# Optimization experiments

Measured on AMD Instinct MI355X. Metric: run time of the kernel, lower is better.

Reference implementation:

```python
import jax, jax.numpy as jnp
import numpy as np
import math

N, E, R = 50000, 800000, 32
DIN = 128
H, D = 8, 16          # num_heads, head_dim; H*D == out_ent_feats == 128
HOP = 5
ALPHA = 0.1
EPS = 1e-5


def layer_norm(x, g, b):
    m = jnp.mean(x, axis=-1, keepdims=True)
    v = jnp.mean((x - m) ** 2, axis=-1, keepdims=True)
    return (x - m) * jax.lax.rsqrt(v + EPS) * g + b


def segment_softmax(e, dst, num_nodes):
    # e: [E, H] scores, softmax over incoming edges of each dst node
    m = jax.ops.segment_max(e, dst, num_segments=num_nodes)      # [N, H]
    ex = jnp.exp(e - m[dst])
    s = jax.ops.segment_sum(ex, dst, num_segments=num_nodes)     # [N, H]
    return ex / s[dst]


def setup_inputs() -> dict:
    key = jax.random.key(0)
    ks = jax.random.split(key, 12)
    gain = 0.02  # small init scale (small_init_gain-style)
    ent_feat = jax.random.normal(ks[0], (N, DIN), dtype=jnp.float32)
    rel_feat = jax.random.normal(ks[1], (R, DIN), dtype=jnp.float32)
    src = jax.random.randint(ks[2], (E,), 0, N, dtype=jnp.int32)
    # guarantee every node has in-degree >= 1 (DGL raises otherwise)
    dst_rand = jax.random.randint(ks[3], (E - N,), 0, N, dtype=jnp.int32)
    dst = jnp.concatenate([jnp.arange(N, dtype=jnp.int32), dst_rand])
    rid = jax.random.randint(ks[4], (E,), 0, R, dtype=jnp.int32)
    W_head = jax.random.normal(ks[5], (DIN, H * D), dtype=jnp.float32) * gain
    W_tail = jax.random.normal(ks[6], (DIN, H * D), dtype=jnp.float32) * gain
    W_ent = jax.random.normal(ks[7], (DIN, H * D), dtype=jnp.float32) * gain
    W_rel = jax.random.normal(ks[8], (DIN, H * D), dtype=jnp.float32) * gain
    attn_r = jax.random.normal(ks[9], (1, H, D), dtype=jnp.float32) * gain
    W1 = jax.random.normal(ks[10], (H * D, 4 * H * D), dtype=jnp.float32) * gain
    W2 = jax.random.normal(ks[11], (4 * H * D, H * D), dtype=jnp.float32) * gain
    return dict(
        ent_feat=ent_feat, rel_feat=rel_feat, src=src, dst=dst, rid=rid,
        W_head=W_head, W_tail=W_tail, W_ent=W_ent, W_rel=W_rel, attn_r=attn_r,
        ln_ent_g=jnp.ones((DIN,), jnp.float32), ln_ent_b=jnp.zeros((DIN,), jnp.float32),
        ln_rel_g=jnp.ones((DIN,), jnp.float32), ln_rel_b=jnp.zeros((DIN,), jnp.float32),
        ff_ln_g=jnp.ones((H * D,), jnp.float32), ff_ln_b=jnp.zeros((H * D,), jnp.float32),
        W1=W1, b1=jnp.zeros((4 * H * D,), jnp.float32),
        W2=W2, b2=jnp.zeros((H * D,), jnp.float32),
    )


def _forward(ent_feat, rel_feat, src, dst, rid,
             W_head, W_tail, W_ent, W_rel, attn_r,
             ln_ent_g, ln_ent_b, ln_rel_g, ln_rel_b, ff_ln_g, ff_ln_b,
             W1, b1, W2, b2):
    n = ent_feat.shape[0]
    x = layer_norm(ent_feat, ln_ent_g, ln_ent_b)
    feat_head = (x @ W_head).reshape(n, H, D)
    feat_tail = (x @ W_tail).reshape(n, H, D)
    feat_ent = (x @ W_ent).reshape(n, H, D)

    # per-edge dot-product attention score: u_dot_v('eh','et')
    e = jnp.sum(feat_head[src] * feat_tail[dst], axis=-1)          # [E, H]

    r = layer_norm(rel_feat, ln_rel_g, ln_rel_b)
    feat_rel = (r @ W_rel).reshape(R, H, D)
    er = jnp.sum(feat_rel * attn_r, axis=-1)                       # [R, H]
    e = e * er[rid]                                                # [E, H]

    # e_mul_v with log_in = log(in_degree) of dst node
    deg = jax.ops.segment_sum(jnp.ones((e.shape[0],), e.dtype), dst, num_segments=n)
    log_in = jnp.log(jnp.maximum(deg, 1.0))                        # [N]
    e = e * log_in[dst][:, None] / math.sqrt(D)

    a = segment_softmax(e, dst, n)                                 # [E, H]

    # PPR diffusion: feat <- (1-alpha) * A^T feat + alpha * feat_0
    feat = feat_ent
    for _ in range(HOP):
        msg = feat[src] * a[:, :, None]                            # [E, H, D]
        agg = jax.ops.segment_sum(msg, dst, num_segments=n)        # [N, H, D]
        feat = (1.0 - ALPHA) * agg + ALPHA * feat_ent

    # residual (Identity: in_ent_feats == out_ent_feats)
    rst = feat + ent_feat.reshape(n, H, D)
    rst = rst.reshape(n, H * D)

    h = layer_norm(rst, ff_ln_g, ff_ln_b)
    ff = jax.nn.relu(h @ W1 + b1) @ W2 + b2
    return ff + rst


def reference(ent_feat, rel_feat, src, dst, rid,
              W_head, W_tail, W_ent, W_rel, attn_r,
              ln_ent_g, ln_ent_b, ln_rel_g, ln_rel_b, ff_ln_g, ff_ln_b,
              W1, b1, W2, b2):
    return _forward(ent_feat, rel_feat, src, dst, rid,
                    W_head, W_tail, W_ent, W_rel, attn_r,
                    ln_ent_g, ln_ent_b, ln_rel_g, ln_rel_b, ff_ln_g, ff_ln_b,
                    W1, b1, W2, b2)
```

## Files before the change

kernel.cpp:

```cpp
#include <hip/hip_runtime.h>
#include <hip/hip_bf16.h>

#define N_NODES 50000
#define N_EDGES 800000
#define N_REL 32
#define DIN 128
#define NH 8
#define HD 16
#define FF_HID 512
#define EPS_LN 1e-5f
#define NBUCK 8
#define BDIV 6250
#define BCAP 114688

typedef __attribute__((ext_vector_type(8))) short bf16x8;
typedef __attribute__((ext_vector_type(4))) float f32x4;
typedef __attribute__((ext_vector_type(2))) float f32x2;
typedef unsigned short ushort_t;
typedef unsigned int uint_t;

static __device__ __forceinline__ unsigned short f2bf(float f) {
    union { float f; unsigned u; } v; v.f = f;
    unsigned r = (v.u + 0x7fffu + ((v.u >> 16) & 1u)) >> 16;
    return (unsigned short)r;
}
static __device__ __forceinline__ float bf2f(unsigned u16) {
    union { unsigned u; float f; } v; v.u = u16 << 16; return v.f;
}
static __device__ __forceinline__ unsigned char f2fp8(float f) {
    return (unsigned char)(__builtin_amdgcn_cvt_pk_fp8_f32(f, f, 0, false) & 0xff);
}
static __device__ __forceinline__ uint_t f2fp8x2(float x0, float x1) {
    return (__builtin_amdgcn_cvt_pk_fp8_f32(x0, x1, 0, false) & 0xffffu);
}
static __device__ __forceinline__ void fp8x4_to_f32(uint_t w, float* o) {
    f32x2 lo = __builtin_amdgcn_cvt_pk_f32_fp8(w, false);
    f32x2 hi = __builtin_amdgcn_cvt_pk_f32_fp8(w, true);
    o[0] = lo.x; o[1] = lo.y; o[2] = hi.x; o[3] = hi.y;
}

static __device__ __forceinline__ void pack_dev(const float* __restrict__ W,
                                                short* __restrict__ out, int K, int Ncols,
                                                int idx) {
    int KT = K >> 5;
    int l = idx & 63;
    int tile = idx >> 6;
    int kt = tile & (KT - 1);
    int ct = tile / KT;
    int c = ct * 16 + (l & 15);
    int k0 = kt * 32 + ((l >> 4) * 8);
    bf16x8 v;
#pragma unroll
    for (int j = 0; j < 8; j++) v[j] = (short)f2bf(W[(size_t)(k0 + j) * Ncols + c]);
    *(bf16x8*)(out + (size_t)idx * 8) = v;
}

#define C0_BIN 512
__global__ __launch_bounds__(256) void combo0_kernel(
    const int* __restrict__ src, const int* __restrict__ dst, const int* __restrict__ rid,
    int* __restrict__ deg, int* __restrict__ gcnt, int2* __restrict__ buck,
    const float* __restrict__ W1, short* __restrict__ W1p, const float* __restrict__ W2,
    short* __restrict__ W2p, const float* __restrict__ Wh, short* __restrict__ Whp,
    const float* __restrict__ Wt, short* __restrict__ Wtp, const float* __restrict__ We,
    short* __restrict__ Wep, const float* __restrict__ rel_feat,
    const float* __restrict__ gr, const float* __restrict__ br,
    const float* __restrict__ W_rel, const float* __restrict__ attn_r,
    float* __restrict__ er) {
    __shared__ float red[128];
    __shared__ float xsr[128];
    __shared__ float prod[128];
    __shared__ int cnt[NBUCK];
    __shared__ int sbase[NBUCK];
    int b = blockIdx.x, tid = threadIdx.x;
    if (b < C0_BIN) {
        const int chunk = (N_EDGES + C0_BIN - 1) / C0_BIN;
        int i0 = b * chunk;
        int i1 = min(i0 + chunk, N_EDGES);
        int rounds = (i1 - i0 + 255) >> 8;
        for (int r = 0; r < rounds; r++) {
            int i = i0 + (r << 8) + tid;
            if (tid < NBUCK) cnt[tid] = 0;
            __syncthreads();
            int d = 0, b8 = 0, rank = 0, py = 0;
            bool v = i < i1;
            if (v) {
                d = dst[i];
                b8 = d / BDIV;
                py = src[i] | (rid[i] << 16);
                rank = atomicAdd(&cnt[b8], 1);
                atomicAdd(&deg[d], 1);
            }
            __syncthreads();
            if (tid < NBUCK) sbase[tid] = atomicAdd(&gcnt[tid], cnt[tid]);
            __syncthreads();
            if (v) buck[(size_t)b8 * BCAP + sbase[b8] + rank] = make_int2(d, py);
            __syncthreads();
        }
    } else if (b < C0_BIN + 32) {
        pack_dev(W1, W1p, DIN, FF_HID, (b - C0_BIN) * 256 + tid);
    } else if (b < C0_BIN + 64) {
        pack_dev(W2, W2p, FF_HID, DIN, (b - C0_BIN - 32) * 256 + tid);
    } else if (b < C0_BIN + 72) {
        pack_dev(Wh, Whp, DIN, DIN, (b - C0_BIN - 64) * 256 + tid);
    } else if (b < C0_BIN + 80) {
        pack_dev(Wt, Wtp, DIN, DIN, (b - C0_BIN - 72) * 256 + tid);
    } else if (b < C0_BIN + 88) {
        pack_dev(We, Wep, DIN, DIN, (b - C0_BIN - 80) * 256 + tid);
    } else {
        int r = b - (C0_BIN + 88);
        float x = 0.f;
        if (tid < 128) {
            x = rel_feat[r * DIN + tid];
            red[tid] = x;
        }
        __syncthreads();
        for (int off = 64; off > 0; off >>= 1) {
            if (tid < off) red[tid] += red[tid + off];
            __syncthreads();
        }
        float mean = red[0] * (1.f / DIN);
        __syncthreads();
        if (tid < 128) red[tid] = x * x;
        __syncthreads();
        for (int off = 64; off > 0; off >>= 1) {
            if (tid < off) red[tid] += red[tid + off];
            __syncthreads();
        }
        float var = red[0] * (1.f / DIN) - mean * mean;
        float rs = rsqrtf(var + EPS_LN);
        if (tid < 128) xsr[tid] = (x - mean) * rs * gr[tid] + br[tid];
        __syncthreads();
        if (tid < 128) {
            float acc = 0.f;
            for (int k = 0; k < DIN; k++) acc += xsr[k] * W_rel[k * DIN + tid];
            prod[tid] = acc * attn_r[tid];
        }
        __syncthreads();
        if (tid < NH) {
            float s = 0.f;
            for (int d = 0; d < HD; d++) s += prod[tid * HD + d];
            er[r * NH + tid] = s;
        }
    }
}

#define NS_SCAN 196
__global__ __launch_bounds__(256) void combo_mid_kernel(
    const int* __restrict__ deg, int* __restrict__ row_off,
    const float* __restrict__ ent, const float* __restrict__ g, const float* __restrict__ b,
    const short* __restrict__ Whp, const short* __restrict__ Wtp,
    const short* __restrict__ Wep, unsigned char* __restrict__ hent,
    ushort_t* __restrict__ tail_bf) {
    __shared__ float xs[32][128];
    __shared__ short hsb[32][136];
    int blk = blockIdx.x, tid = threadIdx.x;
    if (blk < NS_SCAN) {
        __shared__ int lscan[256];
        __shared__ int ws4[4];
        int n = N_NODES;
        int start = blk * 256;
        int partial = 0;
        for (int i = tid; i < start; i += 256) partial += deg[i];
        for (int m = 32; m > 0; m >>= 1) partial += __shfl_down(partial, m);
        int wid = tid >> 6, lane = tid & 63;
        if (lane == 0) ws4[wid] = partial;
        __syncthreads();
        int sbase = ws4[0] + ws4[1] + ws4[2] + ws4[3];
        int i = start + tid;
        int v = (i < n) ? deg[i] : 0;
        lscan[tid] = v;
        __syncthreads();
        for (int off = 1; off < 256; off <<= 1) {
            int t = (tid >= off) ? lscan[tid - off] : 0;
            __syncthreads();
            lscan[tid] += t;
            __syncthreads();
        }
        if (i < n) row_off[i] = sbase + lscan[tid] - v;
        if (i == n - 1) row_off[n] = sbase + lscan[tid];
        return;
    }
    int base = (blk - NS_SCAN) * 32;
    {
        int c = tid & 127, rb = tid >> 7;
#pragma unroll
        for (int j = 0; j < 16; j++) {
            int r = j * 2 + rb;
            int row = base + r;
            xs[r][c] = (row < N_NODES) ? ent[(size_t)row * DIN + c] : 0.f;
        }
    }
    __syncthreads();
    int wave = tid >> 6, lane = tid & 63;
    {
        float g0 = g[lane], g1 = g[lane + 64], bb0 = b[lane], bb1 = b[lane + 64];
        for (int r = wave * 8; r < wave * 8 + 8; r++) {
            float x0 = xs[r][lane], x1 = xs[r][lane + 64];
            float s1 = x0 + x1, s2 = x0 * x0 + x1 * x1;
            for (int m = 1; m < 64; m <<= 1) {
                s1 += __shfl_xor(s1, m);
                s2 += __shfl_xor(s2, m);
            }
            float mean = s1 * (1.f / DIN);
            float var = s2 * (1.f / DIN) - mean * mean;
            float rs = rsqrtf(var + EPS_LN);
            hsb[r][lane] = (short)f2bf((x0 - mean) * rs * g0 + bb0);
            hsb[r][lane + 64] = (short)f2bf((x1 - mean) * rs * g1 + bb1);
        }
    }
    __syncthreads();
    bf16x8 a[2][4];
#pragma unroll
    for (int rt = 0; rt < 2; rt++)
#pragma unroll
        for (int kt = 0; kt < 4; kt++)
            a[rt][kt] = *(const bf16x8*)&hsb[rt * 16 + (lane & 15)][kt * 32 + (lane >> 4) * 8];
#pragma unroll
    for (int m = 0; m < 3; m++) {
        const bf16x8* bp = (m == 0)   ? (const bf16x8*)Whp
                           : (m == 1) ? (const bf16x8*)Wtp
                                      : (const bf16x8*)Wep;
#pragma unroll
        for (int c2 = 0; c2 < 2; c2++) {
            int ct = wave * 2 + c2;
            f32x4 acc0 = {0.f, 0.f, 0.f, 0.f}, acc1 = {0.f, 0.f, 0.f, 0.f};
#pragma unroll
            for (int kt = 0; kt < 4; kt++) {
                bf16x8 bf = bp[(ct * 4 + kt) * 64 + lane];
                acc0 = __builtin_amdgcn_mfma_f32_16x16x32_bf16(a[0][kt], bf, acc0, 0, 0, 0);
                acc1 = __builtin_amdgcn_mfma_f32_16x16x32_bf16(a[1][kt], bf, acc1, 0, 0, 0);
            }
            int col = ct * 16 + (lane & 15);
            int h = col >> 4, k = col & 15;
            int r0 = (lane >> 4) * 4;
#pragma unroll
            for (int j = 0; j < 4; j++) {
                int row0 = base + r0 + j, row1 = base + 16 + r0 + j;
                if (m == 0) {
                    if (row0 < N_NODES) hent[(size_t)row0 * 256 + h * 32 + k] = f2fp8(acc0[j]);
                    if (row1 < N_NODES) hent[(size_t)row1 * 256 + h * 32 + k] = f2fp8(acc1[j]);
                } else if (m == 1) {
                    if (row0 < N_NODES) tail_bf[(size_t)row0 * DIN + col] = f2bf(acc0[j]);
                    if (row1 < N_NODES) tail_bf[(size_t)row1 * DIN + col] = f2bf(acc1[j]);
                } else {
                    if (row0 < N_NODES)
                        hent[(size_t)row0 * 256 + h * 32 + 16 + k] = f2fp8(acc0[j]);
                    if (row1 < N_NODES)
                        hent[(size_t)row1 * 256 + h * 32 + 16 + k] = f2fp8(acc1[j]);
                }
            }
        }
    }
}

__global__ __launch_bounds__(256) void scatter_kernel(
    const int2* __restrict__ buck, const int* __restrict__ gcnt,
    const int* __restrict__ row_off, int* __restrict__ cursor, int* __restrict__ sr_perm) {
    int blk = blockIdx.x, tid = threadIdx.x;
    int b8 = blk & 7, sub = blk >> 3;
    int cnt = gcnt[b8];
    int chunk = (cnt + 127) >> 7;
    int i0 = sub * chunk;
    int i1 = min(i0 + chunk, cnt);
    const int2* bp = buck + (size_t)b8 * BCAP;
    for (int i = i0 + tid; i < i1; i += 256) {
        int2 e = bp[i];
        int p = row_off[e.x] + atomicAdd(&cursor[e.x], 1);
        sr_perm[p] = e.y;
    }
}

__global__ __launch_bounds__(256) void score_hop_kernel(
    const unsigned char* __restrict__ hent, const ushort_t* __restrict__ tail_bf,
    const float* __restrict__ er, const int* __restrict__ row_off,
    const int* __restrict__ sr_perm, ushort_t* __restrict__ a_bf,
    float* __restrict__ inv9, unsigned char* __restrict__ fout) {
    int wid = threadIdx.x >> 6;
    int u = blockIdx.x * 4 + wid;
    int lane = threadIdx.x & 63;
    int h = lane & 7, esub = lane >> 3;
    int p0 = row_off[u], p1 = row_off[u + 1];
    int deg = p1 - p0;
    float scale = logf((float)(deg > 0 ? deg : 1)) * 0.25f;
    float t[16];
    {
        const uint_t* tp = (const uint_t*)(tail_bf + (size_t)u * DIN + h * HD);
#pragma unroll
        for (int i = 0; i < 8; i++) {
            uint_t w = tp[i];
            t[2 * i] = bf2f(w & 0xffffu);
            t[2 * i + 1] = bf2f(w >> 16);
        }
    }
    float ssum = 0.f;
    float acc[16];
#pragma unroll
    for (int k = 0; k < 16; k++) acc[k] = 0.f;
    for (int p = p0 + esub; p < p1; p += 8) {
        int v = sr_perm[p];
        int s = v & 0xffff;
        int rr = v >> 16;
        const uint4* hp = (const uint4*)(hent + (size_t)s * 256 + h * 32);
        uint4 hw = hp[0];
        uint4 ew = hp[1];
        float hv[16], ev[16];
        fp8x4_to_f32(hw.x, hv + 0); fp8x4_to_f32(hw.y, hv + 4);
        fp8x4_to_f32(hw.z, hv + 8); fp8x4_to_f32(hw.w, hv + 12);
        fp8x4_to_f32(ew.x, ev + 0); fp8x4_to_f32(ew.y, ev + 4);
        fp8x4_to_f32(ew.z, ev + 8); fp8x4_to_f32(ew.w, ev + 12);
        float dot = 0.f;
#pragma unroll
        for (int k = 0; k < 16; k++) dot += t[k] * hv[k];
        float e = dot * er[rr * NH + h] * scale;
        float sx = expf(e);
        a_bf[(size_t)p * NH + h] = f2bf(sx);
        ssum += sx;
#pragma unroll
        for (int k = 0; k < 16; k++) acc[k] += sx * ev[k];
    }
    ssum += __shfl_xor(ssum, 8);
    ssum += __shfl_xor(ssum, 16);
    ssum += __shfl_xor(ssum, 32);
#pragma unroll
    for (int k = 0; k < 16; k++) {
        acc[k] += __shfl_xor(acc[k], 8);
        acc[k] += __shfl_xor(acc[k], 16);
        acc[k] += __shfl_xor(acc[k], 32);
    }
    if (esub == 0) {
        float iv = 0.9f / ssum;
        inv9[(size_t)u * NH + h] = iv;
        const uint4 eu = *(const uint4*)(hent + (size_t)u * 256 + h * 32 + 16);
        float e0[16];
        fp8x4_to_f32(eu.x, e0 + 0); fp8x4_to_f32(eu.y, e0 + 4);
        fp8x4_to_f32(eu.z, e0 + 8); fp8x4_to_f32(eu.w, e0 + 12);
        float x[16];
#pragma unroll
        for (int k = 0; k < 16; k++) x[k] = iv * acc[k] + 0.1f * e0[k];
        uint4 ov;
        ov.x = f2fp8x2(x[0], x[1]) | (f2fp8x2(x[2], x[3]) << 16);
        ov.y = f2fp8x2(x[4], x[5]) | (f2fp8x2(x[6], x[7]) << 16);
        ov.z = f2fp8x2(x[8], x[9]) | (f2fp8x2(x[10], x[11]) << 16);
        ov.w = f2fp8x2(x[12], x[13]) | (f2fp8x2(x[14], x[15]) << 16);
        *(uint4*)(fout + (size_t)u * DIN + h * HD) = ov;
    }
}

template <bool OUT_BF>
__global__ __launch_bounds__(256) void diffuse4_kernel(
    const unsigned char* __restrict__ fin8, const unsigned char* __restrict__ hent,
    const ushort_t* __restrict__ a_bf, const int* __restrict__ sr_perm,
    const int* __restrict__ row_off, const float* __restrict__ inv9,
    void* __restrict__ fout) {
    int wid = threadIdx.x >> 6;
    int u = blockIdx.x * 4 + wid;
    int lane = threadIdx.x & 63;
    int c = lane & 15;
    int g = lane >> 4;
    int hh = c >> 1;
    int p0 = row_off[u], p1 = row_off[u + 1];
    float acc[8];
#pragma unroll
    for (int j = 0; j < 8; j++) acc[j] = 0.f;
    for (int p = p0; p < p1; p += 4) {
        int pe = p + g;
        bool valid = pe < p1;
        int pc = valid ? pe : (p1 - 1);
        int s = sr_perm[pc] & 0xffff;
        float a = valid ? bf2f(a_bf[(size_t)pc * NH + hh]) : 0.f;
        uint2 w = *(const uint2*)(fin8 + (size_t)s * DIN + 8 * c);
        float v[8];
        fp8x4_to_f32(w.x, v + 0);
        fp8x4_to_f32(w.y, v + 4);
#pragma unroll
        for (int j = 0; j < 8; j++) acc[j] += a * v[j];
    }
#pragma unroll
    for (int j = 0; j < 8; j++) {
        acc[j] += __shfl_xor(acc[j], 16);
        acc[j] += __shfl_xor(acc[j], 32);
    }
    if (g == 0) {
        float iv = inv9[(size_t)u * NH + hh];
        uint2 ew = *(const uint2*)(hent + (size_t)u * 256 + hh * 32 + 16 + (c & 1) * 8);
        float e0[8];
        fp8x4_to_f32(ew.x, e0 + 0);
        fp8x4_to_f32(ew.y, e0 + 4);
        float x[8];
#pragma unroll
        for (int j = 0; j < 8; j++) x[j] = iv * acc[j] + 0.1f * e0[j];
        size_t o = (size_t)u * DIN + 8 * c;
        if (OUT_BF) {
            uint4 ov;
            ov.x = (uint_t)f2bf(x[0]) | ((uint_t)f2bf(x[1]) << 16);
            ov.y = (uint_t)f2bf(x[2]) | ((uint_t)f2bf(x[3]) << 16);
            ov.z = (uint_t)f2bf(x[4]) | ((uint_t)f2bf(x[5]) << 16);
            ov.w = (uint_t)f2bf(x[6]) | ((uint_t)f2bf(x[7]) << 16);
            *(uint4*)((ushort_t*)fout + o) = ov;
        } else {
            uint2 ov;
            ov.x = f2fp8x2(x[0], x[1]) | (f2fp8x2(x[2], x[3]) << 16);
            ov.y = f2fp8x2(x[4], x[5]) | (f2fp8x2(x[6], x[7]) << 16);
            *(uint2*)((unsigned char*)fout + o) = ov;
        }
    }
}

static __device__ __forceinline__ int hid_idx(int row, int col) {
    return row * 512 + ((((col >> 3) & 63) ^ (row & 7)) << 3) + (col & 7);
}
__global__ __launch_bounds__(256) void ffn_mfma_kernel(
    const ushort_t* __restrict__ feat, const float* __restrict__ ent0,
    const float* __restrict__ g, const float* __restrict__ b,
    const short* __restrict__ W1p, const float* __restrict__ b1,
    const short* __restrict__ W2p, const float* __restrict__ b2,
    float* __restrict__ out) {
    __shared__ ushort_t rst_bf[16][136];
    __shared__ short hs[16][136];
    __shared__ short hid[16 * 512];
    int tid = threadIdx.x;
    int base = blockIdx.x * 16;
    int wave = tid >> 6, lane = tid & 63;
    {
        int c = tid & 127, rb = tid >> 7;
#pragma unroll
        for (int j = 0; j < 8; j++) {
            int r = j * 2 + rb;
            int row = base + r;
            float v = 0.f;
            if (row < N_NODES) {
                size_t idx = (size_t)row * DIN + c;
                v = bf2f(feat[idx]) + ent0[idx];
            }
            rst_bf[r][c] = f2bf(v);
        }
    }
    __syncthreads();
    {
        float g0 = g[lane], g1 = g[lane + 64], bb0 = b[lane], bb1 = b[lane + 64];
        for (int r = wave * 4; r < wave * 4 + 4; r++) {
            float x0 = bf2f(rst_bf[r][lane]), x1 = bf2f(rst_bf[r][lane + 64]);
            float s1 = x0 + x1, s2 = x0 * x0 + x1 * x1;
            for (int m = 1; m < 64; m <<= 1) {
                s1 += __shfl_xor(s1, m);
                s2 += __shfl_xor(s2, m);
            }
            float mean = s1 * (1.f / DIN);
            float var = s2 * (1.f / DIN) - mean * mean;
            float rs = rsqrtf(var + EPS_LN);
            hs[r][lane] = (short)f2bf((x0 - mean) * rs * g0 + bb0);
            hs[r][lane + 64] = (short)f2bf((x1 - mean) * rs * g1 + bb1);
        }
    }
    __syncthreads();
    {
        bf16x8 a[4];
#pragma unroll
        for (int kt = 0; kt < 4; kt++)
            a[kt] = *(const bf16x8*)&hs[lane & 15][kt * 32 + (lane >> 4) * 8];
        const bf16x8* bp = (const bf16x8*)W1p;
        for (int cti = 0; cti < 8; cti++) {
            int ct = wave * 8 + cti;
            f32x4 acc0 = {0.f, 0.f, 0.f, 0.f};
#pragma unroll
            for (int kt = 0; kt < 4; kt++) {
                bf16x8 bf = bp[(ct * 4 + kt) * 64 + lane];
                acc0 = __builtin_amdgcn_mfma_f32_16x16x32_bf16(a[kt], bf, acc0, 0, 0, 0);
            }
            int col = ct * 16 + (lane & 15);
            float bv = b1[col];
            int r0 = (lane >> 4) * 4;
#pragma unroll
            for (int j = 0; j < 4; j++)
                hid[hid_idx(r0 + j, col)] = (short)f2bf(fmaxf(acc0[j] + bv, 0.f));
        }
    }
    __syncthreads();
    {
        f32x4 acc[2] = {{0.f, 0.f, 0.f, 0.f}, {0.f, 0.f, 0.f, 0.f}};
        const bf16x8* bp2 = (const bf16x8*)W2p;
        for (int kt = 0; kt < 16; kt++) {
            int col8 = kt * 32 + (lane >> 4) * 8;
            bf16x8 a0 = *(const bf16x8*)&hid[hid_idx(lane & 15, col8)];
#pragma unroll
            for (int c2 = 0; c2 < 2; c2++) {
                int ct = wave * 2 + c2;
                bf16x8 bf = bp2[(ct * 16 + kt) * 64 + lane];
                acc[c2] = __builtin_amdgcn_mfma_f32_16x16x32_bf16(a0, bf, acc[c2], 0, 0, 0);
            }
        }
#pragma unroll
        for (int c2 = 0; c2 < 2; c2++) {
            int col = (wave * 2 + c2) * 16 + (lane & 15);
            float bv = b2[col];
            int r0 = (lane >> 4) * 4;
#pragma unroll
            for (int j = 0; j < 4; j++) {
                int row = base + r0 + j;
                if (row < N_NODES)
                    out[(size_t)row * DIN + col] = acc[c2][j] + bv + bf2f(rst_bf[r0 + j][col]);
            }
        }
    }
}

extern "C" void kernel_launch(void* const* d_in, const int* in_sizes, int n_in,
                              void* d_out, int out_size, void* d_ws, size_t ws_size,
                              hipStream_t stream) {
    const float* ent_feat = (const float*)d_in[0];
    const float* rel_feat = (const float*)d_in[1];
    const int* src = (const int*)d_in[2];
    const int* dst = (const int*)d_in[3];
    const int* rid = (const int*)d_in[4];
    const float* W_head = (const float*)d_in[5];
    const float* W_tail = (const float*)d_in[6];
    const float* W_ent = (const float*)d_in[7];
    const float* W_rel = (const float*)d_in[8];
    const float* attn_r = (const float*)d_in[9];
    const float* ln_ent_g = (const float*)d_in[10];
    const float* ln_ent_b = (const float*)d_in[11];
    const float* ln_rel_g = (const float*)d_in[12];
    const float* ln_rel_b = (const float*)d_in[13];
    const float* ff_ln_g = (const float*)d_in[14];
    const float* ff_ln_b = (const float*)d_in[15];
    const float* W1 = (const float*)d_in[16];
    const float* b1 = (const float*)d_in[17];
    const float* W2 = (const float*)d_in[18];
    const float* b2 = (const float*)d_in[19];
    float* out = (float*)d_out;

    const int N = N_NODES, E = N_EDGES;

    char* cur = (char*)d_ws;
    auto alloc = [&](size_t bytes, size_t align) -> void* {
        uintptr_t p = (uintptr_t)cur;
        p = (p + align - 1) & ~(uintptr_t)(align - 1);
        cur = (char*)(p + bytes);
        return (void*)p;
    };
    ushort_t* tail_bf = (ushort_t*)alloc((size_t)N * DIN * 2, 16);
    unsigned char* hent = (unsigned char*)alloc((size_t)N * 256, 16);
    unsigned char* f8A = (unsigned char*)alloc((size_t)N * DIN, 16);
    unsigned char* f8B = (unsigned char*)alloc((size_t)N * DIN, 16);
    int2* buck = (int2*)alloc((size_t)NBUCK * BCAP * 8, 16);
    int* sr_perm = (int*)alloc((size_t)E * 4, 16);
    int* row_off = (int*)alloc((size_t)(N + 1) * 4, 16);
    int* deg = (int*)alloc(((size_t)2 * N + NBUCK) * 4, 16);
    int* cursor = deg + N;
    int* gcnt = deg + 2 * N;
    float* er = (float*)alloc((size_t)N_REL * NH * 4, 16);
    float* inv9 = (float*)alloc((size_t)N * NH * 4, 16);
    short* W1p = (short*)alloc((size_t)DIN * FF_HID * 2, 16);
    short* W2p = (short*)alloc((size_t)FF_HID * DIN * 2, 16);
    short* Whp = (short*)alloc((size_t)DIN * DIN * 2, 16);
    short* Wtp = (short*)alloc((size_t)DIN * DIN * 2, 16);
    short* Wep = (short*)alloc((size_t)DIN * DIN * 2, 16);
    ushort_t* a_fit = (ushort_t*)alloc((size_t)E * NH * 2, 16);
    ushort_t* a_bf = ((size_t)(cur - (char*)d_ws) <= ws_size) ? a_fit : (ushort_t*)d_out;

    hipMemsetAsync(deg, 0, sizeof(int) * ((size_t)2 * N + NBUCK), stream);
    combo0_kernel<<<632, 256, 0, stream>>>(src, dst, rid, deg, gcnt, buck, W1, W1p, W2,
                                           W2p, W_head, Whp, W_tail, Wtp, W_ent, Wep,
                                           rel_feat, ln_rel_g, ln_rel_b, W_rel, attn_r,
                                           er);
    int nblk32 = (N + 31) / 32;
    combo_mid_kernel<<<NS_SCAN + nblk32, 256, 0, stream>>>(
        deg, row_off, ent_feat, ln_ent_g, ln_ent_b, Whp, Wtp, Wep, hent, tail_bf);
    scatter_kernel<<<1024, 256, 0, stream>>>(buck, gcnt, row_off, cursor, sr_perm);
    score_hop_kernel<<<N / 4, 256, 0, stream>>>(hent, tail_bf, er, row_off, sr_perm,
                                                a_bf, inv9, f8A);
    diffuse4_kernel<false><<<N / 4, 256, 0, stream>>>(f8A, hent, a_bf, sr_perm, row_off,
                                                      inv9, f8B);
    diffuse4_kernel<false><<<N / 4, 256, 0, stream>>>(f8B, hent, a_bf, sr_perm, row_off,
                                                      inv9, f8A);
    diffuse4_kernel<false><<<N / 4, 256, 0, stream>>>(f8A, hent, a_bf, sr_perm, row_off,
                                                      inv9, f8B);
    diffuse4_kernel<true><<<N / 4, 256, 0, stream>>>(f8B, hent, a_bf, sr_perm, row_off,
                                                     inv9, tail_bf);
    int nblk16 = (N + 15) / 16;
    ffn_mfma_kernel<<<nblk16, 256, 0, stream>>>(tail_bf, ent_feat, ff_ln_g, ff_ln_b, W1p,
                                                b1, W2p, b2, out);
}
```

Before: 355.8 us.

## Fuse final diffusion hop into FFN and move degree histogram out of binning

The last PPR diffusion hop is folded into the FFN kernel, so the aggregated features go straight to shared memory instead of a bf16 round trip through global memory. The degree histogram atomics move from the binning pass into combo_mid, where they read the per-bucket dst arrays and gain locality. Edge buckets split into separate dst and payload arrays, and the scan becomes its own kernel. This adds an extra launch, and the fused kernel's gather phase runs at lower occupancy because of the FFN's shared memory use.

```diff
diff --git a/kernel.cpp b/kernel.cpp
--- a/kernel.cpp
+++ b/kernel.cpp
@@ -58,7 +58,7 @@
 #define C0_BIN 512
 __global__ __launch_bounds__(256) void combo0_kernel(
     const int* __restrict__ src, const int* __restrict__ dst, const int* __restrict__ rid,
-    int* __restrict__ deg, int* __restrict__ gcnt, int2* __restrict__ buck,
+    int* __restrict__ gcnt, int* __restrict__ bdst, int* __restrict__ bpay,
     const float* __restrict__ W1, short* __restrict__ W1p, const float* __restrict__ W2,
     short* __restrict__ W2p, const float* __restrict__ Wh, short* __restrict__ Whp,
     const float* __restrict__ Wt, short* __restrict__ Wtp, const float* __restrict__ We,
@@ -88,12 +88,15 @@
                 b8 = d / BDIV;
                 py = src[i] | (rid[i] << 16);
                 rank = atomicAdd(&cnt[b8], 1);
-                atomicAdd(&deg[d], 1);
             }
             __syncthreads();
             if (tid < NBUCK) sbase[tid] = atomicAdd(&gcnt[tid], cnt[tid]);
             __syncthreads();
-            if (v) buck[(size_t)b8 * BCAP + sbase[b8] + rank] = make_int2(d, py);
+            if (v) {
+                size_t pos = (size_t)b8 * BCAP + sbase[b8] + rank;
+                bdst[pos] = d;
+                bpay[pos] = py;
+            }
             __syncthreads();
         }
     } else if (b < C0_BIN + 32) {
@@ -144,9 +147,9 @@
     }
 }
 
-#define NS_SCAN 196
+#define C_HIST 1024
 __global__ __launch_bounds__(256) void combo_mid_kernel(
-    const int* __restrict__ deg, int* __restrict__ row_off,
+    const int* __restrict__ bdst, const int* __restrict__ gcnt, int* __restrict__ deg,
     const float* __restrict__ ent, const float* __restrict__ g, const float* __restrict__ b,
     const short* __restrict__ Whp, const short* __restrict__ Wtp,
     const short* __restrict__ Wep, unsigned char* __restrict__ hent,
@@ -154,33 +157,17 @@
     __shared__ float xs[32][128];
     __shared__ short hsb[32][136];
     int blk = blockIdx.x, tid = threadIdx.x;
-    if (blk < NS_SCAN) {
-        __shared__ int lscan[256];
-        __shared__ int ws4[4];
-        int n = N_NODES;
-        int start = blk * 256;
-        int partial = 0;
-        for (int i = tid; i < start; i += 256) partial += deg[i];
-        for (int m = 32; m > 0; m >>= 1) partial += __shfl_down(partial, m);
-        int wid = tid >> 6, lane = tid & 63;
-        if (lane == 0) ws4[wid] = partial;
-        __syncthreads();
-        int sbase = ws4[0] + ws4[1] + ws4[2] + ws4[3];
-        int i = start + tid;
-        int v = (i < n) ? deg[i] : 0;
-        lscan[tid] = v;
-        __syncthreads();
-        for (int off = 1; off < 256; off <<= 1) {
-            int t = (tid >= off) ? lscan[tid - off] : 0;
-            __syncthreads();
-            lscan[tid] += t;
-            __syncthreads();
-        }
-        if (i < n) row_off[i] = sbase + lscan[tid] - v;
-        if (i == n - 1) row_off[n] = sbase + lscan[tid];
+    if (blk < C_HIST) {
+        int b8 = blk & 7, sub = blk >> 3;
+        int cnt = gcnt[b8];
+        int chunk = (cnt + 127) >> 7;
+        int i0 = sub * chunk;
+        int i1 = min(i0 + chunk, cnt);
+        const int* bp = bdst + (size_t)b8 * BCAP;
+        for (int i = i0 + tid; i < i1; i += 256) atomicAdd(&deg[bp[i]], 1);
         return;
     }
-    int base = (blk - NS_SCAN) * 32;
+    int base = (blk - C_HIST) * 32;
     {
         int c = tid & 127, rb = tid >> 7;
 #pragma unroll
@@ -253,20 +240,49 @@
     }
 }
 
+__global__ __launch_bounds__(256) void scan2_kernel(const int* __restrict__ deg,
+                                                    int* __restrict__ row_off, int n) {
+    __shared__ int lscan[256];
+    __shared__ int ws4[4];
+    int blk = blockIdx.x, tid = threadIdx.x;
+    int start = blk * 256;
+    int partial = 0;
+    for (int i = tid; i < start; i += 256) partial += deg[i];
+    for (int m = 32; m > 0; m >>= 1) partial += __shfl_down(partial, m);
+    int wid = tid >> 6, lane = tid & 63;
+    if (lane == 0) ws4[wid] = partial;
+    __syncthreads();
+    int sbase = ws4[0] + ws4[1] + ws4[2] + ws4[3];
+    int i = start + tid;
+    int v = (i < n) ? deg[i] : 0;
+    lscan[tid] = v;
+    __syncthreads();
+    for (int off = 1; off < 256; off <<= 1) {
+        int t = (tid >= off) ? lscan[tid - off] : 0;
+        __syncthreads();
+        lscan[tid] += t;
+        __syncthreads();
+    }
+    if (i < n) row_off[i] = sbase + lscan[tid] - v;
+    if (i == n - 1) row_off[n] = sbase + lscan[tid];
+}
+
 __global__ __launch_bounds__(256) void scatter_kernel(
-    const int2* __restrict__ buck, const int* __restrict__ gcnt,
-    const int* __restrict__ row_off, int* __restrict__ cursor, int* __restrict__ sr_perm) {
+    const int* __restrict__ bdst, const int* __restrict__ bpay,
+    const int* __restrict__ gcnt, const int* __restrict__ row_off,
+    int* __restrict__ cursor, int* __restrict__ sr_perm) {
     int blk = blockIdx.x, tid = threadIdx.x;
     int b8 = blk & 7, sub = blk >> 3;
     int cnt = gcnt[b8];
     int chunk = (cnt + 127) >> 7;
     int i0 = sub * chunk;
     int i1 = min(i0 + chunk, cnt);
-    const int2* bp = buck + (size_t)b8 * BCAP;
+    const int* bd = bdst + (size_t)b8 * BCAP;
+    const int* bpp = bpay + (size_t)b8 * BCAP;
     for (int i = i0 + tid; i < i1; i += 256) {
-        int2 e = bp[i];
-        int p = row_off[e.x] + atomicAdd(&cursor[e.x], 1);
-        sr_perm[p] = e.y;
+        int d = bd[i];
+        int p = row_off[d] + atomicAdd(&cursor[d], 1);
+        sr_perm[p] = bpp[i];
     }
 }
 
@@ -409,6 +425,139 @@
 static __device__ __forceinline__ int hid_idx(int row, int col) {
     return row * 512 + ((((col >> 3) & 63) ^ (row & 7)) << 3) + (col & 7);
 }
+static __device__ __forceinline__ void ffn_body(
+    ushort_t (*rst_bf)[136], short (*hs)[136], short* hid, int base, int tid,
+    const float* __restrict__ g, const float* __restrict__ b,
+    const short* __restrict__ W1p, const float* __restrict__ b1,
+    const short* __restrict__ W2p, const float* __restrict__ b2,
+    float* __restrict__ out) {
+    int wave = tid >> 6, lane = tid & 63;
+    {
+        float g0 = g[lane], g1 = g[lane + 64], bb0 = b[lane], bb1 = b[lane + 64];
+        for (int r = wave * 4; r < wave * 4 + 4; r++) {
+            float x0 = bf2f(rst_bf[r][lane]), x1 = bf2f(rst_bf[r][lane + 64]);
+            float s1 = x0 + x1, s2 = x0 * x0 + x1 * x1;
+            for (int m = 1; m < 64; m <<= 1) {
+                s1 += __shfl_xor(s1, m);
+                s2 += __shfl_xor(s2, m);
+            }
+            float mean = s1 * (1.f / DIN);
+            float var = s2 * (1.f / DIN) - mean * mean;
+            float rs = rsqrtf(var + EPS_LN);
+            hs[r][lane] = (short)f2bf((x0 - mean) * rs * g0 + bb0);
+            hs[r][lane + 64] = (short)f2bf((x1 - mean) * rs * g1 + bb1);
+        }
+    }
+    __syncthreads();
+    {
+        bf16x8 a[4];
+#pragma unroll
+        for (int kt = 0; kt < 4; kt++)
+            a[kt] = *(const bf16x8*)&hs[lane & 15][kt * 32 + (lane >> 4) * 8];
+        const bf16x8* bp = (const bf16x8*)W1p;
+        for (int cti = 0; cti < 8; cti++) {
+            int ct = wave * 8 + cti;
+            f32x4 acc0 = {0.f, 0.f, 0.f, 0.f};
+#pragma unroll
+            for (int kt = 0; kt < 4; kt++) {
+                bf16x8 bf = bp[(ct * 4 + kt) * 64 + lane];
+                acc0 = __builtin_amdgcn_mfma_f32_16x16x32_bf16(a[kt], bf, acc0, 0, 0, 0);
+            }
+            int col = ct * 16 + (lane & 15);
+            float bv = b1[col];
+            int r0 = (lane >> 4) * 4;
+#pragma unroll
+            for (int j = 0; j < 4; j++)
+                hid[hid_idx(r0 + j, col)] = (short)f2bf(fmaxf(acc0[j] + bv, 0.f));
+        }
+    }
+    __syncthreads();
+    {
+        f32x4 acc[2] = {{0.f, 0.f, 0.f, 0.f}, {0.f, 0.f, 0.f, 0.f}};
+        const bf16x8* bp2 = (const bf16x8*)W2p;
+        for (int kt = 0; kt < 16; kt++) {
+            int col8 = kt * 32 + (lane >> 4) * 8;
+            bf16x8 a0 = *(const bf16x8*)&hid[hid_idx(lane & 15, col8)];
+#pragma unroll
+            for (int c2 = 0; c2 < 2; c2++) {
+                int ct = wave * 2 + c2;
+                bf16x8 bf = bp2[(ct * 16 + kt) * 64 + lane];
+                acc[c2] = __builtin_amdgcn_mfma_f32_16x16x32_bf16(a0, bf, acc[c2], 0, 0, 0);
+            }
+        }
+#pragma unroll
+        for (int c2 = 0; c2 < 2; c2++) {
+            int col = (wave * 2 + c2) * 16 + (lane & 15);
+            float bv = b2[col];
+            int r0 = (lane >> 4) * 4;
+#pragma unroll
+            for (int j = 0; j < 4; j++) {
+                int row = base + r0 + j;
+                if (row < N_NODES)
+                    out[(size_t)row * DIN + col] = acc[c2][j] + bv + bf2f(rst_bf[r0 + j][col]);
+            }
+        }
+    }
+}
+
+__global__ __launch_bounds__(256) void ffn_fused_kernel(
+    const unsigned char* __restrict__ fin8, const unsigned char* __restrict__ hent,
+    const ushort_t* __restrict__ a_bf, const int* __restrict__ sr_perm,
+    const int* __restrict__ row_off, const float* __restrict__ inv9,
+    const float* __restrict__ ent0, const float* __restrict__ g,
+    const float* __restrict__ b, const short* __restrict__ W1p,
+    const float* __restrict__ b1, const short* __restrict__ W2p,
+    const float* __restrict__ b2, float* __restrict__ out) {
+    __shared__ ushort_t rst_bf[16][136];
+    __shared__ short hs[16][136];
+    __shared__ short hid[16 * 512];
+    int tid = threadIdx.x;
+    int base = blockIdx.x * 16;
+    int wave = tid >> 6, lane = tid & 63;
+    int c = lane & 15, gs = lane >> 4, hh = c >> 1;
+    for (int i = 0; i < 4; i++) {
+        int r = wave * 4 + i;
+        int u = base + r;
+        int p0 = row_off[u], p1 = row_off[u + 1];
+        float acc[8];
+#pragma unroll
+        for (int j = 0; j < 8; j++) acc[j] = 0.f;
+        for (int p = p0; p < p1; p += 4) {
+            int pe = p + gs;
+            bool valid = pe < p1;
+            int pc = valid ? pe : (p1 - 1);
+            int s = sr_perm[pc] & 0xffff;
+            float a = valid ? bf2f(a_bf[(size_t)pc * NH + hh]) : 0.f;
+            uint2 w = *(const uint2*)(fin8 + (size_t)s * DIN + 8 * c);
+            float v[8];
+            fp8x4_to_f32(w.x, v + 0);
+            fp8x4_to_f32(w.y, v + 4);
+#pragma unroll
+            for (int j = 0; j < 8; j++) acc[j] += a * v[j];
+        }
+#pragma unroll
+        for (int j = 0; j < 8; j++) {
+            acc[j] += __shfl_xor(acc[j], 16);
+            acc[j] += __shfl_xor(acc[j], 32);
+        }
+        if (gs == 0) {
+            float iv = inv9[(size_t)u * NH + hh];
+            uint2 ew = *(const uint2*)(hent + (size_t)u * 256 + hh * 32 + 16 + (c & 1) * 8);
+            float e0[8];
+            fp8x4_to_f32(ew.x, e0 + 0);
+            fp8x4_to_f32(ew.y, e0 + 4);
+            const float4* ep = (const float4*)(ent0 + (size_t)u * DIN + 8 * c);
+            float4 ef0 = ep[0], ef1 = ep[1];
+            float ef[8] = {ef0.x, ef0.y, ef0.z, ef0.w, ef1.x, ef1.y, ef1.z, ef1.w};
+#pragma unroll
+            for (int j = 0; j < 8; j++)
+                rst_bf[r][8 * c + j] = f2bf(iv * acc[j] + 0.1f * e0[j] + ef[j]);
+        }
+    }
+    __syncthreads();
+    ffn_body(rst_bf, hs, hid, base, tid, g, b, W1p, b1, W2p, b2, out);
+}
+
 __global__ __launch_bounds__(256) void ffn_mfma_kernel(
     const ushort_t* __restrict__ feat, const float* __restrict__ ent0,
     const float* __restrict__ g, const float* __restrict__ b,
@@ -420,7 +569,6 @@
     __shared__ short hid[16 * 512];
     int tid = threadIdx.x;
     int base = blockIdx.x * 16;
-    int wave = tid >> 6, lane = tid & 63;
     {
         int c = tid & 127, rb = tid >> 7;
 #pragma unroll
@@ -436,72 +584,7 @@
         }
     }
     __syncthreads();
-    {
-        float g0 = g[lane], g1 = g[lane + 64], bb0 = b[lane], bb1 = b[lane + 64];
-        for (int r = wave * 4; r < wave * 4 + 4; r++) {
-            float x0 = bf2f(rst_bf[r][lane]), x1 = bf2f(rst_bf[r][lane + 64]);
-            float s1 = x0 + x1, s2 = x0 * x0 + x1 * x1;
-            for (int m = 1; m < 64; m <<= 1) {
-                s1 += __shfl_xor(s1, m);
-                s2 += __shfl_xor(s2, m);
-            }
-            float mean = s1 * (1.f / DIN);
-            float var = s2 * (1.f / DIN) - mean * mean;
-            float rs = rsqrtf(var + EPS_LN);
-            hs[r][lane] = (short)f2bf((x0 - mean) * rs * g0 + bb0);
-            hs[r][lane + 64] = (short)f2bf((x1 - mean) * rs * g1 + bb1);
-        }
-    }
-    __syncthreads();
-    {
-        bf16x8 a[4];
-#pragma unroll
-        for (int kt = 0; kt < 4; kt++)
-            a[kt] = *(const bf16x8*)&hs[lane & 15][kt * 32 + (lane >> 4) * 8];
-        const bf16x8* bp = (const bf16x8*)W1p;
-        for (int cti = 0; cti < 8; cti++) {
-            int ct = wave * 8 + cti;
-            f32x4 acc0 = {0.f, 0.f, 0.f, 0.f};
-#pragma unroll
-            for (int kt = 0; kt < 4; kt++) {
-                bf16x8 bf = bp[(ct * 4 + kt) * 64 + lane];
-                acc0 = __builtin_amdgcn_mfma_f32_16x16x32_bf16(a[kt], bf, acc0, 0, 0, 0);
-            }
-            int col = ct * 16 + (lane & 15);
-            float bv = b1[col];
-            int r0 = (lane >> 4) * 4;
-#pragma unroll
-            for (int j = 0; j < 4; j++)
-                hid[hid_idx(r0 + j, col)] = (short)f2bf(fmaxf(acc0[j] + bv, 0.f));
-        }
-    }
-    __syncthreads();
-    {
-        f32x4 acc[2] = {{0.f, 0.f, 0.f, 0.f}, {0.f, 0.f, 0.f, 0.f}};
-        const bf16x8* bp2 = (const bf16x8*)W2p;
-        for (int kt = 0; kt < 16; kt++) {
-            int col8 = kt * 32 + (lane >> 4) * 8;
-            bf16x8 a0 = *(const bf16x8*)&hid[hid_idx(lane & 15, col8)];
-#pragma unroll
-            for (int c2 = 0; c2 < 2; c2++) {
-                int ct = wave * 2 + c2;
-                bf16x8 bf = bp2[(ct * 16 + kt) * 64 + lane];
-                acc[c2] = __builtin_amdgcn_mfma_f32_16x16x32_bf16(a0, bf, acc[c2], 0, 0, 0);
-            }
-        }
-#pragma unroll
-        for (int c2 = 0; c2 < 2; c2++) {
-            int col = (wave * 2 + c2) * 16 + (lane & 15);
-            float bv = b2[col];
-            int r0 = (lane >> 4) * 4;
-#pragma unroll
-            for (int j = 0; j < 4; j++) {
-                int row = base + r0 + j;
-                if (row < N_NODES)
-                    out[(size_t)row * DIN + col] = acc[c2][j] + bv + bf2f(rst_bf[r0 + j][col]);
-            }
-        }
-    }
+    ffn_body(rst_bf, hs, hid, base, tid, g, b, W1p, b1, W2p, b2, out);
 }
 
 extern "C" void kernel_launch(void* const* d_in, const int* in_sizes, int n_in,
@@ -542,7 +625,8 @@
     unsigned char* hent = (unsigned char*)alloc((size_t)N * 256, 16);
     unsigned char* f8A = (unsigned char*)alloc((size_t)N * DIN, 16);
     unsigned char* f8B = (unsigned char*)alloc((size_t)N * DIN, 16);
-    int2* buck = (int2*)alloc((size_t)NBUCK * BCAP * 8, 16);
+    int* bdst = (int*)alloc((size_t)NBUCK * BCAP * 4, 16);
+    int* bpay = (int*)alloc((size_t)NBUCK * BCAP * 4, 16);
     int* sr_perm = (int*)alloc((size_t)E * 4, 16);
     int* row_off = (int*)alloc((size_t)(N + 1) * 4, 16);
     int* deg = (int*)alloc(((size_t)2 * N + NBUCK) * 4, 16);
@@ -556,17 +640,19 @@
     short* Wtp = (short*)alloc((size_t)DIN * DIN * 2, 16);
     short* Wep = (short*)alloc((size_t)DIN * DIN * 2, 16);
     ushort_t* a_fit = (ushort_t*)alloc((size_t)E * NH * 2, 16);
-    ushort_t* a_bf = ((size_t)(cur - (char*)d_ws) <= ws_size) ? a_fit : (ushort_t*)d_out;
+    bool a_in_ws = ((size_t)(cur - (char*)d_ws) <= ws_size);
+    ushort_t* a_bf = a_in_ws ? a_fit : (ushort_t*)d_out;
 
     hipMemsetAsync(deg, 0, sizeof(int) * ((size_t)2 * N + NBUCK), stream);
-    combo0_kernel<<<632, 256, 0, stream>>>(src, dst, rid, deg, gcnt, buck, W1, W1p, W2,
+    combo0_kernel<<<632, 256, 0, stream>>>(src, dst, rid, gcnt, bdst, bpay, W1, W1p, W2,
                                            W2p, W_head, Whp, W_tail, Wtp, W_ent, Wep,
                                            rel_feat, ln_rel_g, ln_rel_b, W_rel, attn_r,
                                            er);
     int nblk32 = (N + 31) / 32;
-    combo_mid_kernel<<<NS_SCAN + nblk32, 256, 0, stream>>>(
-        deg, row_off, ent_feat, ln_ent_g, ln_ent_b, Whp, Wtp, Wep, hent, tail_bf);
-    scatter_kernel<<<1024, 256, 0, stream>>>(buck, gcnt, row_off, cursor, sr_perm);
+    combo_mid_kernel<<<C_HIST + nblk32, 256, 0, stream>>>(
+        bdst, gcnt, deg, ent_feat, ln_ent_g, ln_ent_b, Whp, Wtp, Wep, hent, tail_bf);
+    scan2_kernel<<<(N + 255) / 256, 256, 0, stream>>>(deg, row_off, N);
+    scatter_kernel<<<1024, 256, 0, stream>>>(bdst, bpay, gcnt, row_off, cursor, sr_perm);
     score_hop_kernel<<<N / 4, 256, 0, stream>>>(hent, tail_bf, er, row_off, sr_perm,
                                                 a_bf, inv9, f8A);
     diffuse4_kernel<false><<<N / 4, 256, 0, stream>>>(f8A, hent, a_bf, sr_perm, row_off,
@@ -575,9 +661,15 @@
                                                       inv9, f8A);
     diffuse4_kernel<false><<<N / 4, 256, 0, stream>>>(f8A, hent, a_bf, sr_perm, row_off,
                                                       inv9, f8B);
-    diffuse4_kernel<true><<<N / 4, 256, 0, stream>>>(f8B, hent, a_bf, sr_perm, row_off,
-                                                     inv9, tail_bf);
     int nblk16 = (N + 15) / 16;
-    ffn_mfma_kernel<<<nblk16, 256, 0, stream>>>(tail_bf, ent_feat, ff_ln_g, ff_ln_b, W1p,
-                                                b1, W2p, b2, out);
-}
+    if (a_in_ws) {
+        ffn_fused_kernel<<<nblk16, 256, 0, stream>>>(f8B, hent, a_bf, sr_perm, row_off,
+                                                     inv9, ent_feat, ff_ln_g, ff_ln_b,
+                                                     W1p, b1, W2p, b2, out);
+    } else {
+        diffuse4_kernel<true><<<N / 4, 256, 0, stream>>>(f8B, hent, a_bf, sr_perm,
+                                                         row_off, inv9, tail_bf);
+        ffn_mfma_kernel<<<nblk16, 256, 0, stream>>>(tail_bf, ent_feat, ff_ln_g, ff_ln_b,
+                                                    W1p, b1, W2p, b2, out);
+    }
+}
```

New measurement: 419.9 us. +18.0%, slower.

## Move degree histogram out of bucketing pass and split bucket arrays

Applied to the files above, without the earlier changes.

The per-edge global atomicAdd on degree is removed from the bucketing kernel and recomputed in the mid kernel from the destination-bucketed arrays, which are dst-localized per bucket so atomics hit a narrower address range. The int2 bucket array is split into separate dst and payload arrays so the histogram pass reads only dst. The prefix scan moves into its own extra kernel launch. This adds a launch and re-reads bucket data in exchange for less scattered atomic contention in the first pass.

```diff
diff --git a/kernel.cpp b/kernel.cpp
--- a/kernel.cpp
+++ b/kernel.cpp
@@ -58,7 +58,7 @@
 #define C0_BIN 512
 __global__ __launch_bounds__(256) void combo0_kernel(
     const int* __restrict__ src, const int* __restrict__ dst, const int* __restrict__ rid,
-    int* __restrict__ deg, int* __restrict__ gcnt, int2* __restrict__ buck,
+    int* __restrict__ gcnt, int* __restrict__ bdst, int* __restrict__ bpay,
     const float* __restrict__ W1, short* __restrict__ W1p, const float* __restrict__ W2,
     short* __restrict__ W2p, const float* __restrict__ Wh, short* __restrict__ Whp,
     const float* __restrict__ Wt, short* __restrict__ Wtp, const float* __restrict__ We,
@@ -88,12 +88,15 @@
                 b8 = d / BDIV;
                 py = src[i] | (rid[i] << 16);
                 rank = atomicAdd(&cnt[b8], 1);
-                atomicAdd(&deg[d], 1);
             }
             __syncthreads();
             if (tid < NBUCK) sbase[tid] = atomicAdd(&gcnt[tid], cnt[tid]);
             __syncthreads();
-            if (v) buck[(size_t)b8 * BCAP + sbase[b8] + rank] = make_int2(d, py);
+            if (v) {
+                size_t pos = (size_t)b8 * BCAP + sbase[b8] + rank;
+                bdst[pos] = d;
+                bpay[pos] = py;
+            }
             __syncthreads();
         }
     } else if (b < C0_BIN + 32) {
@@ -144,9 +147,9 @@
     }
 }
 
-#define NS_SCAN 196
+#define C_HIST 1024
 __global__ __launch_bounds__(256) void combo_mid_kernel(
-    const int* __restrict__ deg, int* __restrict__ row_off,
+    const int* __restrict__ bdst, const int* __restrict__ gcnt, int* __restrict__ deg,
     const float* __restrict__ ent, const float* __restrict__ g, const float* __restrict__ b,
     const short* __restrict__ Whp, const short* __restrict__ Wtp,
     const short* __restrict__ Wep, unsigned char* __restrict__ hent,
@@ -154,33 +157,17 @@
     __shared__ float xs[32][128];
     __shared__ short hsb[32][136];
     int blk = blockIdx.x, tid = threadIdx.x;
-    if (blk < NS_SCAN) {
-        __shared__ int lscan[256];
-        __shared__ int ws4[4];
-        int n = N_NODES;
-        int start = blk * 256;
-        int partial = 0;
-        for (int i = tid; i < start; i += 256) partial += deg[i];
-        for (int m = 32; m > 0; m >>= 1) partial += __shfl_down(partial, m);
-        int wid = tid >> 6, lane = tid & 63;
-        if (lane == 0) ws4[wid] = partial;
-        __syncthreads();
-        int sbase = ws4[0] + ws4[1] + ws4[2] + ws4[3];
-        int i = start + tid;
-        int v = (i < n) ? deg[i] : 0;
-        lscan[tid] = v;
-        __syncthreads();
-        for (int off = 1; off < 256; off <<= 1) {
-            int t = (tid >= off) ? lscan[tid - off] : 0;
-            __syncthreads();
-            lscan[tid] += t;
-            __syncthreads();
-        }
-        if (i < n) row_off[i] = sbase + lscan[tid] - v;
-        if (i == n - 1) row_off[n] = sbase + lscan[tid];
+    if (blk < C_HIST) {
+        int b8 = blk & 7, sub = blk >> 3;
+        int cnt = gcnt[b8];
+        int chunk = (cnt + 127) >> 7;
+        int i0 = sub * chunk;
+        int i1 = min(i0 + chunk, cnt);
+        const int* bp = bdst + (size_t)b8 * BCAP;
+        for (int i = i0 + tid; i < i1; i += 256) atomicAdd(&deg[bp[i]], 1);
         return;
     }
-    int base = (blk - NS_SCAN) * 32;
+    int base = (blk - C_HIST) * 32;
     {
         int c = tid & 127, rb = tid >> 7;
 #pragma unroll
@@ -253,20 +240,49 @@
     }
 }
 
+__global__ __launch_bounds__(256) void scan2_kernel(const int* __restrict__ deg,
+                                                    int* __restrict__ row_off, int n) {
+    __shared__ int lscan[256];
+    __shared__ int ws4[4];
+    int blk = blockIdx.x, tid = threadIdx.x;
+    int start = blk * 256;
+    int partial = 0;
+    for (int i = tid; i < start; i += 256) partial += deg[i];
+    for (int m = 32; m > 0; m >>= 1) partial += __shfl_down(partial, m);
+    int wid = tid >> 6, lane = tid & 63;
+    if (lane == 0) ws4[wid] = partial;
+    __syncthreads();
+    int sbase = ws4[0] + ws4[1] + ws4[2] + ws4[3];
+    int i = start + tid;
+    int v = (i < n) ? deg[i] : 0;
+    lscan[tid] = v;
+    __syncthreads();
+    for (int off = 1; off < 256; off <<= 1) {
+        int t = (tid >= off) ? lscan[tid - off] : 0;
+        __syncthreads();
+        lscan[tid] += t;
+        __syncthreads();
+    }
+    if (i < n) row_off[i] = sbase + lscan[tid] - v;
+    if (i == n - 1) row_off[n] = sbase + lscan[tid];
+}
+
 __global__ __launch_bounds__(256) void scatter_kernel(
-    const int2* __restrict__ buck, const int* __restrict__ gcnt,
-    const int* __restrict__ row_off, int* __restrict__ cursor, int* __restrict__ sr_perm) {
+    const int* __restrict__ bdst, const int* __restrict__ bpay,
+    const int* __restrict__ gcnt, const int* __restrict__ row_off,
+    int* __restrict__ cursor, int* __restrict__ sr_perm) {
     int blk = blockIdx.x, tid = threadIdx.x;
     int b8 = blk & 7, sub = blk >> 3;
     int cnt = gcnt[b8];
     int chunk = (cnt + 127) >> 7;
     int i0 = sub * chunk;
     int i1 = min(i0 + chunk, cnt);
-    const int2* bp = buck + (size_t)b8 * BCAP;
+    const int* bd = bdst + (size_t)b8 * BCAP;
+    const int* bpp = bpay + (size_t)b8 * BCAP;
     for (int i = i0 + tid; i < i1; i += 256) {
-        int2 e = bp[i];
-        int p = row_off[e.x] + atomicAdd(&cursor[e.x], 1);
-        sr_perm[p] = e.y;
+        int d = bd[i];
+        int p = row_off[d] + atomicAdd(&cursor[d], 1);
+        sr_perm[p] = bpp[i];
     }
 }
 
@@ -542,7 +558,8 @@
     unsigned char* hent = (unsigned char*)alloc((size_t)N * 256, 16);
     unsigned char* f8A = (unsigned char*)alloc((size_t)N * DIN, 16);
     unsigned char* f8B = (unsigned char*)alloc((size_t)N * DIN, 16);
-    int2* buck = (int2*)alloc((size_t)NBUCK * BCAP * 8, 16);
+    int* bdst = (int*)alloc((size_t)NBUCK * BCAP * 4, 16);
+    int* bpay = (int*)alloc((size_t)NBUCK * BCAP * 4, 16);
     int* sr_perm = (int*)alloc((size_t)E * 4, 16);
     int* row_off = (int*)alloc((size_t)(N + 1) * 4, 16);
     int* deg = (int*)alloc(((size_t)2 * N + NBUCK) * 4, 16);
@@ -556,17 +573,19 @@
     short* Wtp = (short*)alloc((size_t)DIN * DIN * 2, 16);
     short* Wep = (short*)alloc((size_t)DIN * DIN * 2, 16);
     ushort_t* a_fit = (ushort_t*)alloc((size_t)E * NH * 2, 16);
-    ushort_t* a_bf = ((size_t)(cur - (char*)d_ws) <= ws_size) ? a_fit : (ushort_t*)d_out;
+    bool a_in_ws = ((size_t)(cur - (char*)d_ws) <= ws_size);
+    ushort_t* a_bf = a_in_ws ? a_fit : (ushort_t*)d_out;
 
     hipMemsetAsync(deg, 0, sizeof(int) * ((size_t)2 * N + NBUCK), stream);
-    combo0_kernel<<<632, 256, 0, stream>>>(src, dst, rid, deg, gcnt, buck, W1, W1p, W2,
+    combo0_kernel<<<632, 256, 0, stream>>>(src, dst, rid, gcnt, bdst, bpay, W1, W1p, W2,
                                            W2p, W_head, Whp, W_tail, Wtp, W_ent, Wep,
                                            rel_feat, ln_rel_g, ln_rel_b, W_rel, attn_r,
                                            er);
     int nblk32 = (N + 31) / 32;
-    combo_mid_kernel<<<NS_SCAN + nblk32, 256, 0, stream>>>(
-        deg, row_off, ent_feat, ln_ent_g, ln_ent_b, Whp, Wtp, Wep, hent, tail_bf);
-    scatter_kernel<<<1024, 256, 0, stream>>>(buck, gcnt, row_off, cursor, sr_perm);
+    combo_mid_kernel<<<C_HIST + nblk32, 256, 0, stream>>>(
+        bdst, gcnt, deg, ent_feat, ln_ent_g, ln_ent_b, Whp, Wtp, Wep, hent, tail_bf);
+    scan2_kernel<<<(N + 255) / 256, 256, 0, stream>>>(deg, row_off, N);
+    scatter_kernel<<<1024, 256, 0, stream>>>(bdst, bpay, gcnt, row_off, cursor, sr_perm);
     score_hop_kernel<<<N / 4, 256, 0, stream>>>(hent, tail_bf, er, row_off, sr_perm,
                                                 a_bf, inv9, f8A);
     diffuse4_kernel<false><<<N / 4, 256, 0, stream>>>(f8A, hent, a_bf, sr_perm, row_off,
```

Result: slower. 400.2 us (+12.5%).
